# Kernel optimization log

Measured on AMD Instinct MI355X. Metric: run time of the kernel, lower is better.

## Reference

```python
import jax, jax.numpy as jnp
import numpy as np

VOCAB, EMBED, HIDDEN = 29, 64, 256
B, SEQ = 8, 257  # T = SEQ-1 = 256


def setup_inputs() -> dict:
    key = jax.random.key(0)
    ks = jax.random.split(key, 16)
    s = 0.02
    embed = jax.random.normal(ks[0], (VOCAB, EMBED), jnp.float32) * s
    embed = embed.at[0].set(0.0)  # padding_idx = PAD_TOKEN = 0
    d = dict(
        x=jax.random.randint(ks[1], (B, SEQ), 0, VOCAB),
        embed=embed,
        W_ih0=jax.random.normal(ks[2], (HIDDEN, EMBED), jnp.float32) * s,
        b_ih0=jax.random.normal(ks[3], (HIDDEN,), jnp.float32) * s,
        W_hh0=jax.random.normal(ks[4], (HIDDEN, HIDDEN), jnp.float32) * s,
        b_hh0=jax.random.normal(ks[5], (HIDDEN,), jnp.float32) * s,
        W_ih1=jax.random.normal(ks[6], (HIDDEN, HIDDEN), jnp.float32) * s,
        b_ih1=jax.random.normal(ks[7], (HIDDEN,), jnp.float32) * s,
        W_hh1=jax.random.normal(ks[8], (HIDDEN, HIDDEN), jnp.float32) * s,
        b_hh1=jax.random.normal(ks[9], (HIDDEN,), jnp.float32) * s,
        Wq=jax.random.normal(ks[10], (HIDDEN, HIDDEN), jnp.float32) * s,
        Wk=jax.random.normal(ks[11], (HIDDEN, HIDDEN), jnp.float32) * s,
        v=jax.random.normal(ks[12], (HIDDEN,), jnp.float32) * s,
        Wfc=jax.random.normal(ks[13], (VOCAB, 2 * HIDDEN), jnp.float32) * s,
        bfc=jax.random.normal(ks[14], (VOCAB,), jnp.float32) * s,
    )
    return d


def _forward(x, embed, W_ih0, b_ih0, W_hh0, b_hh0, W_ih1, b_ih1, W_hh1, b_hh1,
             Wq, Wk, v, Wfc, bfc):
    inp = x[:, :-1]                       # (B, T)
    emb = embed[inp]                      # (B, T, E); dropout = identity (eval)
    Bb, T, _ = emb.shape
    H = W_hh0.shape[0]

    # 2-layer Elman RNN via scan over time
    def step(carry, e_t):
        h0, h1 = carry
        h0 = jnp.tanh(e_t @ W_ih0.T + b_ih0 + h0 @ W_hh0.T + b_hh0)
        h1 = jnp.tanh(h0 @ W_ih1.T + b_ih1 + h1 @ W_hh1.T + b_hh1)
        return (h0, h1), h1

    init = (jnp.zeros((Bb, H), emb.dtype), jnp.zeros((Bb, H), emb.dtype))
    _, hs = jax.lax.scan(step, init, jnp.swapaxes(emb, 0, 1))  # (T, B, H)
    Hs = jnp.swapaxes(hs, 0, 1)           # (B, T, H) = all_hidden

    # Bahdanau additive self-attention over strictly-past hidden states
    q = Hs @ Wq.T                         # (B, T, H)
    k = Hs @ Wk.T                         # (B, T, H)
    e = jnp.tanh(q[:, :, None, :] + k[:, None, :, :])   # (B, T, T, H)
    scores = jnp.einsum('btsh,h->bts', e, v)             # (B, T, T)
    causal = jnp.tril(jnp.ones((T, T), bool), k=-1)      # s < t strictly
    scores = jnp.where(causal[None], scores, jnp.float32(-1e9))
    alpha = jax.nn.softmax(scores, axis=-1)
    ctx = jnp.einsum('bts,bsh->bth', alpha, Hs)          # (B, T, H)
    ctx = ctx * (jnp.arange(T) > 0)[None, :, None]       # t=0: zero context

    out = jnp.concatenate([Hs, ctx], axis=-1) @ Wfc.T + bfc  # (B, T, V)
    return out


def reference(x, embed, W_ih0, b_ih0, W_hh0, b_hh0, W_ih1, b_ih1, W_hh1, b_hh1,
              Wq, Wk, v, Wfc, bfc):
    return _forward(x, embed, W_ih0, b_ih0, W_hh0, b_hh0, W_ih1, b_ih1,
                    W_hh1, b_hh1, Wq, Wk, v, Wfc, bfc)
```

## Files before the change

kernel.cpp:

```cpp
#include <hip/hip_runtime.h>

#define HID   256
#define BATCH 8
#define TT    256
#define SEQL  257
#define VOCAB 29
#define EMB   64
#define TG    4
#define CH    8
#define NCHK  (TT / CH)

typedef _Float16 f16;
typedef f16  f16x8 __attribute__((ext_vector_type(8)));
typedef float f32x4 __attribute__((ext_vector_type(4)));

__device__ __forceinline__ float fast_tanh(float x) {
    float e = exp2f(x * 2.8853900817779268f);
    return 1.0f - 2.0f * __builtin_amdgcn_rcpf(1.0f + e);
}

__global__ __launch_bounds__(256) void pre0_kernel(
    const int* __restrict__ x, const float* __restrict__ embed,
    const float* __restrict__ Wih0, const float* __restrict__ bih0,
    const float* __restrict__ bhh0, float* __restrict__ C0, int* __restrict__ flags)
{
    if (blockIdx.x == 0 && threadIdx.x < 16) flags[threadIdx.x] = 0;
    int b  = blockIdx.x & 7;
    int t0 = (blockIdx.x >> 3) * 8;
    int tid = threadIdx.x;
    __shared__ float er[8][EMB];
    for (int idx = tid; idx < 8 * EMB; idx += 256) {
        int tt = idx >> 6, j = idx & 63;
        er[tt][j] = embed[x[b * SEQL + t0 + tt] * EMB + j];
    }
    __syncthreads();
    int i = tid;
    float base = bih0[i] + bhh0[i];
    float acc[8];
#pragma unroll
    for (int tt = 0; tt < 8; ++tt) acc[tt] = base;
    const float* wr = Wih0 + i * EMB;
    for (int j = 0; j < EMB; j += 4) {
        float4 w = *(const float4*)&wr[j];
#pragma unroll
        for (int tt = 0; tt < 8; ++tt) {
            float4 h = *(const float4*)&er[tt][j];
            acc[tt] += h.x * w.x + h.y * w.y + h.z * w.z + h.w * w.w;
        }
    }
#pragma unroll
    for (int tt = 0; tt < 8; ++tt)
        C0[((t0 + tt) * BATCH + b) * HID + i] = acc[tt];
}

__global__ __launch_bounds__(512) void rec3_kernel(
    const float* __restrict__ Whh0, const float* __restrict__ Wih1,
    const float* __restrict__ Whh1, const float* __restrict__ bih1,
    const float* __restrict__ bhh1, const float* __restrict__ C0,
    f16* __restrict__ H0h, float* __restrict__ C1,
    float* __restrict__ Hs, int* __restrict__ flags)
{
    __shared__ f16 hbuf[2][HID];
    __shared__ __align__(16) f16 stg[CH][HID];
    int tid = threadIdx.x;
    int wave = tid >> 6, lane = tid & 63;
    int lrow = lane & 15, lkg = lane >> 4;
    int role = blockIdx.x >> 3;
    int b = blockIdx.x & 7;
    int i0 = wave * 32 + lrow, i1 = i0 + 16;
    const f32x4 Z = {0.f, 0.f, 0.f, 0.f};

    f16x8 a[8];
#pragma unroll
    for (int kt = 0; kt < 8; ++kt)
#pragma unroll
        for (int e = 0; e < 8; ++e) a[kt][e] = (f16)0.f;

    if (role == 0) {
        for (int idx = tid; idx < 2 * HID; idx += 512) ((f16*)hbuf)[idx] = (f16)0.f;
        f16x8 bf[8][2];
#pragma unroll
        for (int kt = 0; kt < 8; ++kt)
#pragma unroll
            for (int ct = 0; ct < 2; ++ct) {
                int n = wave * 32 + ct * 16 + lrow;
                const float* src = Whh0 + n * HID + kt * 32 + lkg * 8;
                f16x8 v;
#pragma unroll
                for (int e = 0; e < 8; ++e) v[e] = (f16)src[e];
                bf[kt][ct] = v;
            }
        __syncthreads();

        const float* cp = C0 + b * HID;
        float c0 = cp[i0], c1 = cp[i1];
        cp += BATCH * HID;
        f16* hp = H0h + (size_t)b * TT * HID;

#define ASTEP(CUR, NXT)                                                             \
    {                                                                               \
        float cn0 = cp[i0];                                                         \
        float cn1 = cp[i1];                                                         \
        cp += BATCH * HID;                                                          \
        if (lrow == 0) {                                                            \
            _Pragma("unroll")                                                       \
            for (int kt = 0; kt < 8; ++kt)                                          \
                a[kt] = *(const f16x8*)&hbuf[CUR][kt * 32 + lkg * 8];               \
        }                                                                           \
        f32x4 p00 = __builtin_amdgcn_mfma_f32_16x16x32_f16(a[0], bf[0][0], Z, 0, 0, 0); \
        f32x4 p01 = __builtin_amdgcn_mfma_f32_16x16x32_f16(a[0], bf[0][1], Z, 0, 0, 0); \
        f32x4 p10 = __builtin_amdgcn_mfma_f32_16x16x32_f16(a[2], bf[2][0], Z, 0, 0, 0); \
        f32x4 p11 = __builtin_amdgcn_mfma_f32_16x16x32_f16(a[2], bf[2][1], Z, 0, 0, 0); \
        f32x4 p20 = __builtin_amdgcn_mfma_f32_16x16x32_f16(a[4], bf[4][0], Z, 0, 0, 0); \
        f32x4 p21 = __builtin_amdgcn_mfma_f32_16x16x32_f16(a[4], bf[4][1], Z, 0, 0, 0); \
        f32x4 p30 = __builtin_amdgcn_mfma_f32_16x16x32_f16(a[6], bf[6][0], Z, 0, 0, 0); \
        f32x4 p31 = __builtin_amdgcn_mfma_f32_16x16x32_f16(a[6], bf[6][1], Z, 0, 0, 0); \
        p00 = __builtin_amdgcn_mfma_f32_16x16x32_f16(a[1], bf[1][0], p00, 0, 0, 0); \
        p01 = __builtin_amdgcn_mfma_f32_16x16x32_f16(a[1], bf[1][1], p01, 0, 0, 0); \
        p10 = __builtin_amdgcn_mfma_f32_16x16x32_f16(a[3], bf[3][0], p10, 0, 0, 0); \
        p11 = __builtin_amdgcn_mfma_f32_16x16x32_f16(a[3], bf[3][1], p11, 0, 0, 0); \
        p20 = __builtin_amdgcn_mfma_f32_16x16x32_f16(a[5], bf[5][0], p20, 0, 0, 0); \
        p21 = __builtin_amdgcn_mfma_f32_16x16x32_f16(a[5], bf[5][1], p21, 0, 0, 0); \
        p30 = __builtin_amdgcn_mfma_f32_16x16x32_f16(a[7], bf[7][0], p30, 0, 0, 0); \
        p31 = __builtin_amdgcn_mfma_f32_16x16x32_f16(a[7], bf[7][1], p31, 0, 0, 0); \
        float v0 = fast_tanh(((p00[0] + p10[0]) + (p20[0] + p30[0])) + c0);         \
        float v1 = fast_tanh(((p01[0] + p11[0]) + (p21[0] + p31[0])) + c1);         \
        f16 hv0 = (f16)v0, hv1 = (f16)v1;                                           \
        if (lane < 16) {                                                            \
            hbuf[NXT][i0] = hv0;                                                    \
            hbuf[NXT][i1] = hv1;                                                    \
            hp[i0] = hv0;                                                           \
            hp[i1] = hv1;                                                           \
        }                                                                           \
        hp += HID;                                                                  \
        c0 = cn0; c1 = cn1;                                                         \
        asm volatile("s_waitcnt lgkmcnt(0)\n\ts_barrier" ::: "memory");             \
    }

        for (int ch = 0; ch < NCHK; ++ch) {
            ASTEP(0, 1) ASTEP(1, 0) ASTEP(0, 1) ASTEP(1, 0)
            ASTEP(0, 1) ASTEP(1, 0) ASTEP(0, 1) ASTEP(1, 0)
            __syncthreads();
            if (tid == 0) {
                __threadfence();
                __hip_atomic_store(&flags[b], ch + 1, __ATOMIC_RELEASE, __HIP_MEMORY_SCOPE_AGENT);
            }
        }
#undef ASTEP
    } else if (role == 1) {
        f16x8 bfI[8][2];
#pragma unroll
        for (int kt = 0; kt < 8; ++kt)
#pragma unroll
            for (int ct = 0; ct < 2; ++ct) {
                int n = wave * 32 + ct * 16 + lrow;
                const float* src = Wih1 + n * HID + kt * 32 + lkg * 8;
                f16x8 v;
#pragma unroll
                for (int e = 0; e < 8; ++e) v[e] = (f16)src[e];
                bfI[kt][ct] = v;
            }
        int col0 = wave * 32 + (lane & 15), col1 = col0 + 16;
        float bv0 = bih1[col0] + bhh1[col0];
        float bv1 = bih1[col1] + bhh1[col1];
        const f16* hsrc = H0h + (size_t)b * TT * HID;
        float* cbase = C1 + (size_t)b * TT * HID;

        for (int ch = 0; ch < NCHK; ++ch) {
            if (tid == 0) {
                while (__hip_atomic_load(&flags[b], __ATOMIC_ACQUIRE, __HIP_MEMORY_SCOPE_AGENT) < ch + 1)
                    __builtin_amdgcn_s_sleep(2);
            }
            __syncthreads();
            if (tid < 256)
                *(f16x8*)((f16*)stg + tid * 8) =
                    *(const f16x8*)(hsrc + (size_t)ch * CH * HID + tid * 8);
            __syncthreads();
            if (lrow < 8) {
#pragma unroll
                for (int kt = 0; kt < 8; ++kt)
                    a[kt] = *(const f16x8*)&stg[lrow][kt * 32 + lkg * 8];
            }
            f32x4 u0 = __builtin_amdgcn_mfma_f32_16x16x32_f16(a[0], bfI[0][0], Z, 0, 0, 0);
            f32x4 u1 = __builtin_amdgcn_mfma_f32_16x16x32_f16(a[0], bfI[0][1], Z, 0, 0, 0);
#pragma unroll
            for (int kt = 1; kt < 8; ++kt) {
                u0 = __builtin_amdgcn_mfma_f32_16x16x32_f16(a[kt], bfI[kt][0], u0, 0, 0, 0);
                u1 = __builtin_amdgcn_mfma_f32_16x16x32_f16(a[kt], bfI[kt][1], u1, 0, 0, 0);
            }
            if (lane < 32) {
                float* co = cbase + (size_t)(ch * CH + (lane >> 4) * 4) * HID;
                co[0 * HID + col0] = u0[0] + bv0;
                co[1 * HID + col0] = u0[1] + bv0;
                co[2 * HID + col0] = u0[2] + bv0;
                co[3 * HID + col0] = u0[3] + bv0;
                co[0 * HID + col1] = u1[0] + bv1;
                co[1 * HID + col1] = u1[1] + bv1;
                co[2 * HID + col1] = u1[2] + bv1;
                co[3 * HID + col1] = u1[3] + bv1;
            }
            __syncthreads();
            if (tid == 0) {
                __threadfence();
                __hip_atomic_store(&flags[8 + b], ch + 1, __ATOMIC_RELEASE, __HIP_MEMORY_SCOPE_AGENT);
            }
        }
    } else {
        for (int idx = tid; idx < 2 * HID; idx += 512) ((f16*)hbuf)[idx] = (f16)0.f;
        f16x8 bf[8][2];
#pragma unroll
        for (int kt = 0; kt < 8; ++kt)
#pragma unroll
            for (int ct = 0; ct < 2; ++ct) {
                int n = wave * 32 + ct * 16 + lrow;
                const float* src = Whh1 + n * HID + kt * 32 + lkg * 8;
                f16x8 v;
#pragma unroll
                for (int e = 0; e < 8; ++e) v[e] = (f16)src[e];
                bf[kt][ct] = v;
            }
        __syncthreads();
        float* ho = Hs + (size_t)b * TT * HID;
        const float* cq = C1 + (size_t)b * TT * HID;

#define CSTEP(CUR, NXT, CV0, CV1)                                                   \
    {                                                                               \
        if (lrow == 0) {                                                            \
            _Pragma("unroll")                                                       \
            for (int kt = 0; kt < 8; ++kt)                                          \
                a[kt] = *(const f16x8*)&hbuf[CUR][kt * 32 + lkg * 8];               \
        }                                                                           \
        f32x4 p00 = __builtin_amdgcn_mfma_f32_16x16x32_f16(a[0], bf[0][0], Z, 0, 0, 0); \
        f32x4 p01 = __builtin_amdgcn_mfma_f32_16x16x32_f16(a[0], bf[0][1], Z, 0, 0, 0); \
        f32x4 p10 = __builtin_amdgcn_mfma_f32_16x16x32_f16(a[2], bf[2][0], Z, 0, 0, 0); \
        f32x4 p11 = __builtin_amdgcn_mfma_f32_16x16x32_f16(a[2], bf[2][1], Z, 0, 0, 0); \
        f32x4 p20 = __builtin_amdgcn_mfma_f32_16x16x32_f16(a[4], bf[4][0], Z, 0, 0, 0); \
        f32x4 p21 = __builtin_amdgcn_mfma_f32_16x16x32_f16(a[4], bf[4][1], Z, 0, 0, 0); \
        f32x4 p30 = __builtin_amdgcn_mfma_f32_16x16x32_f16(a[6], bf[6][0], Z, 0, 0, 0); \
        f32x4 p31 = __builtin_amdgcn_mfma_f32_16x16x32_f16(a[6], bf[6][1], Z, 0, 0, 0); \
        p00 = __builtin_amdgcn_mfma_f32_16x16x32_f16(a[1], bf[1][0], p00, 0, 0, 0); \
        p01 = __builtin_amdgcn_mfma_f32_16x16x32_f16(a[1], bf[1][1], p01, 0, 0, 0); \
        p10 = __builtin_amdgcn_mfma_f32_16x16x32_f16(a[3], bf[3][0], p10, 0, 0, 0); \
        p11 = __builtin_amdgcn_mfma_f32_16x16x32_f16(a[3], bf[3][1], p11, 0, 0, 0); \
        p20 = __builtin_amdgcn_mfma_f32_16x16x32_f16(a[5], bf[5][0], p20, 0, 0, 0); \
        p21 = __builtin_amdgcn_mfma_f32_16x16x32_f16(a[5], bf[5][1], p21, 0, 0, 0); \
        p30 = __builtin_amdgcn_mfma_f32_16x16x32_f16(a[7], bf[7][0], p30, 0, 0, 0); \
        p31 = __builtin_amdgcn_mfma_f32_16x16x32_f16(a[7], bf[7][1], p31, 0, 0, 0); \
        float v0 = fast_tanh(((p00[0] + p10[0]) + (p20[0] + p30[0])) + CV0);        \
        float v1 = fast_tanh(((p01[0] + p11[0]) + (p21[0] + p31[0])) + CV1);        \
        if (lane < 16) {                                                            \
            hbuf[NXT][i0] = (f16)v0;                                                \
            hbuf[NXT][i1] = (f16)v1;                                                \
            ho[i0] = v0;                                                            \
            ho[i1] = v1;                                                            \
        }                                                                           \
        ho += HID;                                                                  \
        asm volatile("s_waitcnt lgkmcnt(0)\n\ts_barrier" ::: "memory");             \
    }

        for (int ch = 0; ch < NCHK; ++ch) {
            if (tid == 0) {
                while (__hip_atomic_load(&flags[8 + b], __ATOMIC_ACQUIRE, __HIP_MEMORY_SCOPE_AGENT) < ch + 1)
                    __builtin_amdgcn_s_sleep(2);
            }
            __syncthreads();
            const float* cc = cq + (size_t)ch * CH * HID;
            float d00 = cc[0*HID+i0], d01 = cc[0*HID+i1];
            float d10 = cc[1*HID+i0], d11 = cc[1*HID+i1];
            float d20 = cc[2*HID+i0], d21 = cc[2*HID+i1];
            float d30 = cc[3*HID+i0], d31 = cc[3*HID+i1];
            float d40 = cc[4*HID+i0], d41 = cc[4*HID+i1];
            float d50 = cc[5*HID+i0], d51 = cc[5*HID+i1];
            float d60 = cc[6*HID+i0], d61 = cc[6*HID+i1];
            float d70 = cc[7*HID+i0], d71 = cc[7*HID+i1];
            CSTEP(0, 1, d00, d01) CSTEP(1, 0, d10, d11)
            CSTEP(0, 1, d20, d21) CSTEP(1, 0, d30, d31)
            CSTEP(0, 1, d40, d41) CSTEP(1, 0, d50, d51)
            CSTEP(0, 1, d60, d61) CSTEP(1, 0, d70, d71)
        }
#undef CSTEP
    }
}

__global__ __launch_bounds__(256) void gemmqk_kernel(
    const float* __restrict__ In, const float* __restrict__ Wq,
    const float* __restrict__ Wk, float* __restrict__ Oq, float* __restrict__ OkT)
{
    int b  = blockIdx.x & 7;
    int t0 = (blockIdx.x >> 3) * 8;
    int tid = threadIdx.x;
    __shared__ float hs[8][HID];
    for (int idx = tid; idx < 8 * HID; idx += 256) {
        int tt = idx >> 8, j = idx & 255;
        hs[tt][j] = In[((size_t)b * TT + t0 + tt) * HID + j];
    }
    __syncthreads();
    int i = tid;
    float aq[8], ak[8];
#pragma unroll
    for (int tt = 0; tt < 8; ++tt) { aq[tt] = 0.f; ak[tt] = 0.f; }
    const float* wq = Wq + i * HID;
    const float* wk = Wk + i * HID;
    for (int j = 0; j < HID; j += 4) {
        float4 q = *(const float4*)&wq[j];
        float4 k = *(const float4*)&wk[j];
#pragma unroll
        for (int tt = 0; tt < 8; ++tt) {
            float4 h = *(const float4*)&hs[tt][j];
            aq[tt] += h.x * q.x + h.y * q.y + h.z * q.z + h.w * q.w;
            ak[tt] += h.x * k.x + h.y * k.y + h.z * k.z + h.w * k.w;
        }
    }
#pragma unroll
    for (int tt = 0; tt < 8; ++tt)
        Oq[((size_t)b * TT + t0 + tt) * HID + i] = fast_tanh(aq[tt]);
    float4 kv0 = { fast_tanh(ak[0]), fast_tanh(ak[1]), fast_tanh(ak[2]), fast_tanh(ak[3]) };
    float4 kv1 = { fast_tanh(ak[4]), fast_tanh(ak[5]), fast_tanh(ak[6]), fast_tanh(ak[7]) };
    float* ko = OkT + ((size_t)b * HID + i) * TT + t0;
    *(float4*)&ko[0] = kv0;
    *(float4*)&ko[4] = kv1;
}

__global__ __launch_bounds__(256) void attn_kernel(
    const float* __restrict__ tq, const float* __restrict__ tkT,
    const float* __restrict__ vvec, const float* __restrict__ Hs,
    const float* __restrict__ Wfc, const float* __restrict__ bfc,
    float* __restrict__ out)
{
    int b  = blockIdx.x & 7;
    int t0 = (blockIdx.x >> 3) * TG;
    int tid = threadIdx.x;
    int wave = tid >> 6, lane = tid & 63;
    __shared__ float qs[TG][HID], vs[HID], alpha[TG][HID];
    __shared__ float cvec[TG][8][68];
    __shared__ float redm[4][TG], reds[4][TG];
#pragma unroll
    for (int j = 0; j < TG; ++j)
        qs[j][tid] = tq[((size_t)b * TT + t0 + j) * HID + tid];
    vs[tid] = vvec[tid];
    __syncthreads();

    float sc[TG];
#pragma unroll
    for (int j = 0; j < TG; ++j) sc[j] = -1e30f;
    if ((wave << 6) < t0 + TG) {
        const float* kT = tkT + (size_t)b * HID * TT + tid;
        float a0 = 0.f, a1 = 0.f, a2 = 0.f, a3 = 0.f;
        for (int jj = 0; jj < HID; jj += 4) {
            float k0 = kT[(size_t)(jj + 0) * TT];
            float k1 = kT[(size_t)(jj + 1) * TT];
            float k2 = kT[(size_t)(jj + 2) * TT];
            float k3 = kT[(size_t)(jj + 3) * TT];
            float4 vv = *(const float4*)&vs[jj];
            float4 q0 = *(const float4*)&qs[0][jj];
            float4 q1 = *(const float4*)&qs[1][jj];
            float4 q2 = *(const float4*)&qs[2][jj];
            float4 q3 = *(const float4*)&qs[3][jj];
#define TADD(qc, kc, vc, acc) { float num = qc + kc; float den = __builtin_fmaf(qc, kc, 1.f); acc += vc * num * __builtin_amdgcn_rcpf(den); }
            TADD(q0.x, k0, vv.x, a0) TADD(q0.y, k1, vv.y, a0) TADD(q0.z, k2, vv.z, a0) TADD(q0.w, k3, vv.w, a0)
            TADD(q1.x, k0, vv.x, a1) TADD(q1.y, k1, vv.y, a1) TADD(q1.z, k2, vv.z, a1) TADD(q1.w, k3, vv.w, a1)
            TADD(q2.x, k0, vv.x, a2) TADD(q2.y, k1, vv.y, a2) TADD(q2.z, k2, vv.z, a2) TADD(q2.w, k3, vv.w, a2)
            TADD(q3.x, k0, vv.x, a3) TADD(q3.y, k1, vv.y, a3) TADD(q3.z, k2, vv.z, a3) TADD(q3.w, k3, vv.w, a3)
#undef TADD
        }
        if (tid < t0 + 0) sc[0] = a0;
        if (tid < t0 + 1) sc[1] = a1;
        if (tid < t0 + 2) sc[2] = a2;
        if (tid < t0 + 3) sc[3] = a3;
    }
    float m0 = sc[0], m1 = sc[1], m2 = sc[2], m3 = sc[3];
#pragma unroll
    for (int off = 32; off; off >>= 1) {
        m0 = fmaxf(m0, __shfl_down(m0, off));
        m1 = fmaxf(m1, __shfl_down(m1, off));
        m2 = fmaxf(m2, __shfl_down(m2, off));
        m3 = fmaxf(m3, __shfl_down(m3, off));
    }
    if (lane == 0) { redm[wave][0] = m0; redm[wave][1] = m1; redm[wave][2] = m2; redm[wave][3] = m3; }
    __syncthreads();
    float ej[TG];
#pragma unroll
    for (int j = 0; j < TG; ++j) {
        float m = fmaxf(fmaxf(redm[0][j], redm[1][j]), fmaxf(redm[2][j], redm[3][j]));
        ej[j] = (tid < t0 + j) ? exp2f((sc[j] - m) * 1.4426950408889634f) : 0.f;
    }
    float z0 = ej[0], z1 = ej[1], z2 = ej[2], z3 = ej[3];
#pragma unroll
    for (int off = 32; off; off >>= 1) {
        z0 += __shfl_down(z0, off);
        z1 += __shfl_down(z1, off);
        z2 += __shfl_down(z2, off);
        z3 += __shfl_down(z3, off);
    }
    if (lane == 0) { reds[wave][0] = z0; reds[wave][1] = z1; reds[wave][2] = z2; reds[wave][3] = z3; }
    __syncthreads();
#pragma unroll
    for (int j = 0; j < TG; ++j) {
        float z = reds[0][j] + reds[1][j] + reds[2][j] + reds[3][j];
        alpha[j][tid] = (t0 + j == 0) ? 0.f : ej[j] * __builtin_amdgcn_rcpf(z);
    }
    __syncthreads();

    float c0 = 0.f, c1 = 0.f, c2 = 0.f, c3 = 0.f;
    const float* hb = Hs + (size_t)b * TT * HID;
    for (int s = 0; s < t0 + TG; s += 4) {
        float4 av0 = *(const float4*)&alpha[0][s];
        float4 av1 = *(const float4*)&alpha[1][s];
        float4 av2 = *(const float4*)&alpha[2][s];
        float4 av3 = *(const float4*)&alpha[3][s];
        float h0 = hb[(s + 0) * HID + tid];
        float h1 = hb[(s + 1) * HID + tid];
        float h2 = hb[(s + 2) * HID + tid];
        float h3 = hb[(s + 3) * HID + tid];
        c0 += av0.x * h0 + av0.y * h1 + av0.z * h2 + av0.w * h3;
        c1 += av1.x * h0 + av1.y * h1 + av1.z * h2 + av1.w * h3;
        c2 += av2.x * h0 + av2.y * h1 + av2.z * h2 + av2.w * h3;
        c3 += av3.x * h0 + av3.y * h1 + av3.z * h2 + av3.w * h3;
    }
    {
        int ph = tid >> 6, jj = tid & 63;
        cvec[0][ph][jj] = hb[(size_t)(t0 + 0) * HID + tid]; cvec[0][4 + ph][jj] = c0;
        cvec[1][ph][jj] = hb[(size_t)(t0 + 1) * HID + tid]; cvec[1][4 + ph][jj] = c1;
        cvec[2][ph][jj] = hb[(size_t)(t0 + 2) * HID + tid]; cvec[2][4 + ph][jj] = c2;
        cvec[3][ph][jj] = hb[(size_t)(t0 + 3) * HID + tid]; cvec[3][4 + ph][jj] = c3;
    }
    __syncthreads();

    if (tid < VOCAB * 8) {
        int o = tid >> 3, p = tid & 7;
        const float* wr = Wfc + o * 2 * HID + p * 64;
#pragma unroll
        for (int j = 0; j < TG; ++j) {
            const float* cv = &cvec[j][p][0];
            float a = 0.f;
            for (int jj = 0; jj < 64; jj += 4) {
                float4 w  = *(const float4*)&wr[jj];
                float4 cc = *(const float4*)&cv[jj];
                a += w.x * cc.x + w.y * cc.y + w.z * cc.z + w.w * cc.w;
            }
            a += __shfl_down(a, 4);
            a += __shfl_down(a, 2);
            a += __shfl_down(a, 1);
            if (p == 0) out[((size_t)b * TT + t0 + j) * VOCAB + o] = a + bfc[o];
        }
    }
}

extern "C" void kernel_launch(void* const* d_in, const int* in_sizes, int n_in,
                              void* d_out, int out_size, void* d_ws, size_t ws_size,
                              hipStream_t stream)
{
    (void)in_sizes; (void)n_in; (void)out_size; (void)ws_size;
    const int*   x     = (const int*)d_in[0];
    const float* embed = (const float*)d_in[1];
    const float* Wih0  = (const float*)d_in[2];
    const float* bih0  = (const float*)d_in[3];
    const float* Whh0  = (const float*)d_in[4];
    const float* bhh0  = (const float*)d_in[5];
    const float* Wih1  = (const float*)d_in[6];
    const float* bih1  = (const float*)d_in[7];
    const float* Whh1  = (const float*)d_in[8];
    const float* bhh1  = (const float*)d_in[9];
    const float* Wq    = (const float*)d_in[10];
    const float* Wk    = (const float*)d_in[11];
    const float* vvec  = (const float*)d_in[12];
    const float* Wfc   = (const float*)d_in[13];
    const float* bfc   = (const float*)d_in[14];
    float* out = (float*)d_out;
    float* ws  = (float*)d_ws;

    const size_t SZ = (size_t)TT * BATCH * HID;
    float* C0   = ws;
    float* Hs   = ws + SZ;
    float* C1   = ws + 2 * SZ;
    f16*   H0h  = (f16*)(ws + 3 * SZ);
    int*   flags = (int*)(ws + 3 * SZ + SZ / 2);
    float* tq   = ws;
    float* tkT  = ws + 2 * SZ;

    pre0_kernel<<<256, 256, 0, stream>>>(x, embed, Wih0, bih0, bhh0, C0, flags);
    rec3_kernel<<<24, 512, 0, stream>>>(Whh0, Wih1, Whh1, bih1, bhh1, C0, H0h, C1, Hs, flags);
    gemmqk_kernel<<<256, 256, 0, stream>>>(Hs, Wq, Wk, tq, tkT);
    attn_kernel<<<512, 256, 0, stream>>>(tq, tkT, vvec, Hs, Wfc, bfc, out);
}
```

Baseline: 240.1 us.

## Fuse embedding projection, recurrence and Q/K projections into one flag-pipelined kernel

Merges the layer-0 input projection, the three recurrence roles and the Q/K projection GEMM into a single 48-block kernel. Roles hand work to each other per 8-step chunk through global flags, so the input projection and the Q/K projections overlap with the serial recurrence instead of running as separate launches before and after it. The Q/K projection now uses fp16 MFMA instead of fp32 scalar FMAs. This adds cross-block spin-waits, and Q-buffer reuse means H0 in fp16, C1 and Q share memory with interleaved strides. The flags live in the output buffer and are cleared by a memset.

After: 243.1 us. No clear change (+1.2%).

```diff
diff --git a/kernel.cpp b/kernel.cpp
--- a/kernel.cpp
+++ b/kernel.cpp
@@ -19,49 +19,19 @@
     return 1.0f - 2.0f * __builtin_amdgcn_rcpf(1.0f + e);
 }
 
-__global__ __launch_bounds__(256) void pre0_kernel(
+__global__ __launch_bounds__(512) void mega_kernel(
     const int* __restrict__ x, const float* __restrict__ embed,
     const float* __restrict__ Wih0, const float* __restrict__ bih0,
-    const float* __restrict__ bhh0, float* __restrict__ C0, int* __restrict__ flags)
-{
-    if (blockIdx.x == 0 && threadIdx.x < 16) flags[threadIdx.x] = 0;
-    int b  = blockIdx.x & 7;
-    int t0 = (blockIdx.x >> 3) * 8;
-    int tid = threadIdx.x;
-    __shared__ float er[8][EMB];
-    for (int idx = tid; idx < 8 * EMB; idx += 256) {
-        int tt = idx >> 6, j = idx & 63;
-        er[tt][j] = embed[x[b * SEQL + t0 + tt] * EMB + j];
-    }
-    __syncthreads();
-    int i = tid;
-    float base = bih0[i] + bhh0[i];
-    float acc[8];
-#pragma unroll
-    for (int tt = 0; tt < 8; ++tt) acc[tt] = base;
-    const float* wr = Wih0 + i * EMB;
-    for (int j = 0; j < EMB; j += 4) {
-        float4 w = *(const float4*)&wr[j];
-#pragma unroll
-        for (int tt = 0; tt < 8; ++tt) {
-            float4 h = *(const float4*)&er[tt][j];
-            acc[tt] += h.x * w.x + h.y * w.y + h.z * w.z + h.w * w.w;
-        }
-    }
-#pragma unroll
-    for (int tt = 0; tt < 8; ++tt)
-        C0[((t0 + tt) * BATCH + b) * HID + i] = acc[tt];
-}
-
-__global__ __launch_bounds__(512) void rec3_kernel(
-    const float* __restrict__ Whh0, const float* __restrict__ Wih1,
-    const float* __restrict__ Whh1, const float* __restrict__ bih1,
-    const float* __restrict__ bhh1, const float* __restrict__ C0,
-    f16* __restrict__ H0h, float* __restrict__ C1,
-    float* __restrict__ Hs, int* __restrict__ flags)
+    const float* __restrict__ bhh0, const float* __restrict__ Whh0,
+    const float* __restrict__ Wih1, const float* __restrict__ Whh1,
+    const float* __restrict__ bih1, const float* __restrict__ bhh1,
+    const float* __restrict__ Wq, const float* __restrict__ Wk,
+    float* __restrict__ C0, float* __restrict__ Q,
+    float* __restrict__ Hs, float* __restrict__ tkT, int* __restrict__ flags)
 {
     __shared__ f16 hbuf[2][HID];
     __shared__ __align__(16) f16 stg[CH][HID];
+    __shared__ float er[CH][EMB];
     int tid = threadIdx.x;
     int wave = tid >> 6, lane = tid & 63;
     int lrow = lane & 15, lkg = lane >> 4;
@@ -70,6 +40,25 @@
     int i0 = wave * 32 + lrow, i1 = i0 + 16;
     const f32x4 Z = {0.f, 0.f, 0.f, 0.f};
 
+#define WAITF(idx, val)                                                             \
+    {                                                                               \
+        if (tid == 0) {                                                             \
+            while (__hip_atomic_load(&flags[idx], __ATOMIC_ACQUIRE,                 \
+                                     __HIP_MEMORY_SCOPE_AGENT) < (val))             \
+                __builtin_amdgcn_s_sleep(2);                                        \
+        }                                                                           \
+        __syncthreads();                                                            \
+    }
+#define POSTF(idx, val)                                                             \
+    {                                                                               \
+        __syncthreads();                                                            \
+        if (tid == 0) {                                                             \
+            __threadfence();                                                        \
+            __hip_atomic_store(&flags[idx], (val), __ATOMIC_RELEASE,                \
+                               __HIP_MEMORY_SCOPE_AGENT);                           \
+        }                                                                           \
+    }
+
     f16x8 a[8];
 #pragma unroll
     for (int kt = 0; kt < 8; ++kt)
@@ -77,6 +66,33 @@
         for (int e = 0; e < 8; ++e) a[kt][e] = (f16)0.f;
 
     if (role == 0) {
+        int i = tid & 255, half = tid >> 8;
+        float base = bih0[i] + bhh0[i];
+        const float* wr = Wih0 + i * EMB;
+        for (int ch = 0; ch < NCHK; ++ch) {
+            int tb = ch * CH;
+            { int tt = tid >> 6, j = tid & 63;
+              er[tt][j] = embed[x[b * SEQL + tb + tt] * EMB + j]; }
+            __syncthreads();
+            float a0 = base, a1 = base, a2 = base, a3 = base;
+            for (int j = 0; j < EMB; j += 4) {
+                float4 w = *(const float4*)&wr[j];
+                float4 h0 = *(const float4*)&er[half * 4 + 0][j];
+                float4 h1 = *(const float4*)&er[half * 4 + 1][j];
+                float4 h2 = *(const float4*)&er[half * 4 + 2][j];
+                float4 h3 = *(const float4*)&er[half * 4 + 3][j];
+                a0 += h0.x * w.x + h0.y * w.y + h0.z * w.z + h0.w * w.w;
+                a1 += h1.x * w.x + h1.y * w.y + h1.z * w.z + h1.w * w.w;
+                a2 += h2.x * w.x + h2.y * w.y + h2.z * w.z + h2.w * w.w;
+                a3 += h3.x * w.x + h3.y * w.y + h3.z * w.z + h3.w * w.w;
+            }
+            C0[((size_t)(tb + half * 4 + 0) * BATCH + b) * HID + i] = a0;
+            C0[((size_t)(tb + half * 4 + 1) * BATCH + b) * HID + i] = a1;
+            C0[((size_t)(tb + half * 4 + 2) * BATCH + b) * HID + i] = a2;
+            C0[((size_t)(tb + half * 4 + 3) * BATCH + b) * HID + i] = a3;
+            POSTF(b, ch + 1)
+        }
+    } else if (role == 1) {
         for (int idx = tid; idx < 2 * HID; idx += 512) ((f16*)hbuf)[idx] = (f16)0.f;
         f16x8 bf[8][2];
 #pragma unroll
@@ -91,11 +107,9 @@
                 bf[kt][ct] = v;
             }
         __syncthreads();
-
         const float* cp = C0 + b * HID;
-        float c0 = cp[i0], c1 = cp[i1];
-        cp += BATCH * HID;
-        f16* hp = H0h + (size_t)b * TT * HID;
+        float c0 = 0.f, c1 = 0.f;
+        f16* hp = (f16*)(Q + (size_t)b * TT * HID);
 
 #define ASTEP(CUR, NXT)                                                             \
     {                                                                               \
@@ -132,22 +146,20 @@
             hp[i0] = hv0;                                                           \
             hp[i1] = hv1;                                                           \
         }                                                                           \
-        hp += HID;                                                                  \
+        hp += 2 * HID;                                                              \
         c0 = cn0; c1 = cn1;                                                         \
         asm volatile("s_waitcnt lgkmcnt(0)\n\ts_barrier" ::: "memory");             \
     }
 
         for (int ch = 0; ch < NCHK; ++ch) {
+            WAITF(b, (ch + 2 < NCHK) ? ch + 2 : NCHK)
+            if (ch == 0) { c0 = cp[i0]; c1 = cp[i1]; cp += BATCH * HID; }
             ASTEP(0, 1) ASTEP(1, 0) ASTEP(0, 1) ASTEP(1, 0)
             ASTEP(0, 1) ASTEP(1, 0) ASTEP(0, 1) ASTEP(1, 0)
-            __syncthreads();
-            if (tid == 0) {
-                __threadfence();
-                __hip_atomic_store(&flags[b], ch + 1, __ATOMIC_RELEASE, __HIP_MEMORY_SCOPE_AGENT);
-            }
+            POSTF(8 + b, ch + 1)
         }
 #undef ASTEP
-    } else if (role == 1) {
+    } else if (role == 2) {
         f16x8 bfI[8][2];
 #pragma unroll
         for (int kt = 0; kt < 8; ++kt)
@@ -163,18 +175,15 @@
         int col0 = wave * 32 + (lane & 15), col1 = col0 + 16;
         float bv0 = bih1[col0] + bhh1[col0];
         float bv1 = bih1[col1] + bhh1[col1];
-        const f16* hsrc = H0h + (size_t)b * TT * HID;
-        float* cbase = C1 + (size_t)b * TT * HID;
+        float* qb = Q + (size_t)b * TT * HID;
 
         for (int ch = 0; ch < NCHK; ++ch) {
-            if (tid == 0) {
-                while (__hip_atomic_load(&flags[b], __ATOMIC_ACQUIRE, __HIP_MEMORY_SCOPE_AGENT) < ch + 1)
-                    __builtin_amdgcn_s_sleep(2);
-            }
-            __syncthreads();
-            if (tid < 256)
-                *(f16x8*)((f16*)stg + tid * 8) =
-                    *(const f16x8*)(hsrc + (size_t)ch * CH * HID + tid * 8);
+            WAITF(8 + b, ch + 1)
+            if (tid < 256) {
+                int tp = tid >> 5, seg = tid & 31;
+                *(f16x8*)&stg[tp][seg * 8] =
+                    *(const f16x8*)((const f16*)(qb + (size_t)(ch * CH + tp) * HID) + seg * 8);
+            }
             __syncthreads();
             if (lrow < 8) {
 #pragma unroll
@@ -189,7 +198,7 @@
                 u1 = __builtin_amdgcn_mfma_f32_16x16x32_f16(a[kt], bfI[kt][1], u1, 0, 0, 0);
             }
             if (lane < 32) {
-                float* co = cbase + (size_t)(ch * CH + (lane >> 4) * 4) * HID;
+                float* co = qb + (size_t)(ch * CH + (lane >> 4) * 4) * HID;
                 co[0 * HID + col0] = u0[0] + bv0;
                 co[1 * HID + col0] = u0[1] + bv0;
                 co[2 * HID + col0] = u0[2] + bv0;
@@ -199,13 +208,9 @@
                 co[2 * HID + col1] = u1[2] + bv1;
                 co[3 * HID + col1] = u1[3] + bv1;
             }
-            __syncthreads();
-            if (tid == 0) {
-                __threadfence();
-                __hip_atomic_store(&flags[8 + b], ch + 1, __ATOMIC_RELEASE, __HIP_MEMORY_SCOPE_AGENT);
-            }
-        }
-    } else {
+            POSTF(16 + b, ch + 1)
+        }
+    } else if (role == 3) {
         for (int idx = tid; idx < 2 * HID; idx += 512) ((f16*)hbuf)[idx] = (f16)0.f;
         f16x8 bf[8][2];
 #pragma unroll
@@ -221,7 +226,7 @@
             }
         __syncthreads();
         float* ho = Hs + (size_t)b * TT * HID;
-        const float* cq = C1 + (size_t)b * TT * HID;
+        const float* cq = Q + (size_t)b * TT * HID;
 
 #define CSTEP(CUR, NXT, CV0, CV1)                                                   \
     {                                                                               \
@@ -259,11 +264,7 @@
     }
 
         for (int ch = 0; ch < NCHK; ++ch) {
-            if (tid == 0) {
-                while (__hip_atomic_load(&flags[8 + b], __ATOMIC_ACQUIRE, __HIP_MEMORY_SCOPE_AGENT) < ch + 1)
-                    __builtin_amdgcn_s_sleep(2);
-            }
-            __syncthreads();
+            WAITF(16 + b, ch + 1)
             const float* cc = cq + (size_t)ch * CH * HID;
             float d00 = cc[0*HID+i0], d01 = cc[0*HID+i1];
             float d10 = cc[1*HID+i0], d11 = cc[1*HID+i1];
@@ -277,48 +278,76 @@
             CSTEP(0, 1, d20, d21) CSTEP(1, 0, d30, d31)
             CSTEP(0, 1, d40, d41) CSTEP(1, 0, d50, d51)
             CSTEP(0, 1, d60, d61) CSTEP(1, 0, d70, d71)
+            POSTF(24 + b, ch + 1)
         }
 #undef CSTEP
-    }
-}
-
-__global__ __launch_bounds__(256) void gemmqk_kernel(
-    const float* __restrict__ In, const float* __restrict__ Wq,
-    const float* __restrict__ Wk, float* __restrict__ Oq, float* __restrict__ OkT)
-{
-    int b  = blockIdx.x & 7;
-    int t0 = (blockIdx.x >> 3) * 8;
-    int tid = threadIdx.x;
-    __shared__ float hs[8][HID];
-    for (int idx = tid; idx < 8 * HID; idx += 256) {
-        int tt = idx >> 8, j = idx & 255;
-        hs[tt][j] = In[((size_t)b * TT + t0 + tt) * HID + j];
-    }
-    __syncthreads();
-    int i = tid;
-    float aq[8], ak[8];
-#pragma unroll
-    for (int tt = 0; tt < 8; ++tt) { aq[tt] = 0.f; ak[tt] = 0.f; }
-    const float* wq = Wq + i * HID;
-    const float* wk = Wk + i * HID;
-    for (int j = 0; j < HID; j += 4) {
-        float4 q = *(const float4*)&wq[j];
-        float4 k = *(const float4*)&wk[j];
-#pragma unroll
-        for (int tt = 0; tt < 8; ++tt) {
-            float4 h = *(const float4*)&hs[tt][j];
-            aq[tt] += h.x * q.x + h.y * q.y + h.z * q.z + h.w * q.w;
-            ak[tt] += h.x * k.x + h.y * k.y + h.z * k.z + h.w * k.w;
-        }
-    }
-#pragma unroll
-    for (int tt = 0; tt < 8; ++tt)
-        Oq[((size_t)b * TT + t0 + tt) * HID + i] = fast_tanh(aq[tt]);
-    float4 kv0 = { fast_tanh(ak[0]), fast_tanh(ak[1]), fast_tanh(ak[2]), fast_tanh(ak[3]) };
-    float4 kv1 = { fast_tanh(ak[4]), fast_tanh(ak[5]), fast_tanh(ak[6]), fast_tanh(ak[7]) };
-    float* ko = OkT + ((size_t)b * HID + i) * TT + t0;
-    *(float4*)&ko[0] = kv0;
-    *(float4*)&ko[4] = kv1;
+    } else {
+        const float* W = (role == 4) ? Wq : Wk;
+        f16x8 bfW[8][2];
+#pragma unroll
+        for (int kt = 0; kt < 8; ++kt)
+#pragma unroll
+            for (int ct = 0; ct < 2; ++ct) {
+                int n = wave * 32 + ct * 16 + lrow;
+                const float* src = W + n * HID + kt * 32 + lkg * 8;
+                f16x8 v;
+#pragma unroll
+                for (int e = 0; e < 8; ++e) v[e] = (f16)src[e];
+                bfW[kt][ct] = v;
+            }
+        int col0 = wave * 32 + (lane & 15), col1 = col0 + 16;
+        const float* hsb = Hs + (size_t)b * TT * HID;
+        float* qb = Q + (size_t)b * TT * HID;
+
+        for (int ch = 0; ch < NCHK; ++ch) {
+            WAITF(24 + b, ch + 1)
+            if (tid < 256) {
+                const float* src = hsb + (size_t)ch * CH * HID + tid * 8;
+                float4 v0 = *(const float4*)&src[0];
+                float4 v1 = *(const float4*)&src[4];
+                f16x8 h = { (f16)v0.x, (f16)v0.y, (f16)v0.z, (f16)v0.w,
+                            (f16)v1.x, (f16)v1.y, (f16)v1.z, (f16)v1.w };
+                *(f16x8*)((f16*)stg + tid * 8) = h;
+            }
+            __syncthreads();
+            if (lrow < 8) {
+#pragma unroll
+                for (int kt = 0; kt < 8; ++kt)
+                    a[kt] = *(const f16x8*)&stg[lrow][kt * 32 + lkg * 8];
+            }
+            f32x4 u0 = __builtin_amdgcn_mfma_f32_16x16x32_f16(a[0], bfW[0][0], Z, 0, 0, 0);
+            f32x4 u1 = __builtin_amdgcn_mfma_f32_16x16x32_f16(a[0], bfW[0][1], Z, 0, 0, 0);
+#pragma unroll
+            for (int kt = 1; kt < 8; ++kt) {
+                u0 = __builtin_amdgcn_mfma_f32_16x16x32_f16(a[kt], bfW[kt][0], u0, 0, 0, 0);
+                u1 = __builtin_amdgcn_mfma_f32_16x16x32_f16(a[kt], bfW[kt][1], u1, 0, 0, 0);
+            }
+            if (lane < 32) {
+                int tb2 = ch * CH + (lane >> 4) * 4;
+                if (role == 4) {
+                    float* co = qb + (size_t)tb2 * HID;
+                    co[0 * HID + col0] = fast_tanh(u0[0]);
+                    co[1 * HID + col0] = fast_tanh(u0[1]);
+                    co[2 * HID + col0] = fast_tanh(u0[2]);
+                    co[3 * HID + col0] = fast_tanh(u0[3]);
+                    co[0 * HID + col1] = fast_tanh(u1[0]);
+                    co[1 * HID + col1] = fast_tanh(u1[1]);
+                    co[2 * HID + col1] = fast_tanh(u1[2]);
+                    co[3 * HID + col1] = fast_tanh(u1[3]);
+                } else {
+                    float4 s0 = { fast_tanh(u0[0]), fast_tanh(u0[1]),
+                                  fast_tanh(u0[2]), fast_tanh(u0[3]) };
+                    float4 s1 = { fast_tanh(u1[0]), fast_tanh(u1[1]),
+                                  fast_tanh(u1[2]), fast_tanh(u1[3]) };
+                    *(float4*)&tkT[((size_t)b * HID + col0) * TT + tb2] = s0;
+                    *(float4*)&tkT[((size_t)b * HID + col1) * TT + tb2] = s1;
+                }
+            }
+            __syncthreads();
+        }
+    }
+#undef WAITF
+#undef POSTF
 }
 
 __global__ __launch_bounds__(256) void attn_kernel(
@@ -470,16 +499,15 @@
     float* ws  = (float*)d_ws;
 
     const size_t SZ = (size_t)TT * BATCH * HID;
-    float* C0   = ws;
-    float* Hs   = ws + SZ;
-    float* C1   = ws + 2 * SZ;
-    f16*   H0h  = (f16*)(ws + 3 * SZ);
-    int*   flags = (int*)(ws + 3 * SZ + SZ / 2);
-    float* tq   = ws;
-    float* tkT  = ws + 2 * SZ;
-
-    pre0_kernel<<<256, 256, 0, stream>>>(x, embed, Wih0, bih0, bhh0, C0, flags);
-    rec3_kernel<<<24, 512, 0, stream>>>(Whh0, Wih1, Whh1, bih1, bhh1, C0, H0h, C1, Hs, flags);
-    gemmqk_kernel<<<256, 256, 0, stream>>>(Hs, Wq, Wk, tq, tkT);
-    attn_kernel<<<512, 256, 0, stream>>>(tq, tkT, vvec, Hs, Wfc, bfc, out);
+    float* C0  = ws;
+    float* Hs  = ws + SZ;
+    float* Q   = ws + 2 * SZ;
+    float* tkT = ws + 3 * SZ;
+    int* flags = (int*)d_out;
+
+    hipMemsetAsync(flags, 0, 32 * sizeof(int), stream);
+    mega_kernel<<<48, 512, 0, stream>>>(x, embed, Wih0, bih0, bhh0, Whh0,
+                                        Wih1, Whh1, bih1, bhh1, Wq, Wk,
+                                        C0, Q, Hs, tkT, flags);
+    attn_kernel<<<512, 256, 0, stream>>>(Q, tkT, vvec, Hs, Wfc, bfc, out);
 }
```
